# Kernel optimization log

Measured on AMD Instinct MI355X. Metric: run time of the kernel, lower is better.

Reference implementation:

```python
import jax, jax.numpy as jnp
import numpy as np

B, N = 8, 6                 # batch, cameras
D, C = 45, 64               # depth bins, context channels
FH, FW = 8, 22              # feature-map height/width
GX, GY, GZ = 64, 64, 32     # BEV grid: W, H, D in the torch code
RES = 0.5
XOFF, YOFF, ZOFF = 16.0, 16.0, 8.0


def _frustum():
    # matches LSS.create_frustum: pixel coords over full 352x128 image, depths 1..45
    xs = jnp.linspace(0.0, 351.0, FW)
    ys = jnp.linspace(0.0, 127.0, FH)
    ds = jnp.arange(1.0, 46.0, 1.0)
    d, y, x = jnp.meshgrid(ds, ys, xs, indexing='ij')   # [D, FH, FW]
    return jnp.stack([x * d, y * d, d], axis=-1)         # [D, FH, FW, 3]


def setup_inputs() -> dict:
    key = jax.random.key(0)
    k1, k2, k3 = jax.random.split(key, 3)
    # depthNet output: softmax over depth bins
    depth = jax.nn.softmax(jax.random.normal(k1, (B, N, D, FH, FW), dtype=jnp.float32), axis=2)
    feature = jax.random.normal(k2, (B, N, C, FH, FW), dtype=jnp.float32)
    # realistic pinhole intrinsics (invertible), identity rotations, small translations
    K = jnp.array([[250.0, 0.0, 176.0], [0.0, 250.0, 64.0], [0.0, 0.0, 1.0]], dtype=jnp.float32)
    intrinsics = jnp.tile(K, (B, N, 1, 1))
    rots = jnp.tile(jnp.eye(3, dtype=jnp.float32), (B, N, 1, 1))
    trans = jax.random.normal(k3, (B, N, 3), dtype=jnp.float32) * 0.5
    return {"depth": depth, "feature": feature, "rots": rots, "trans": trans, "intrinsics": intrinsics}


def reference(depth, feature, rots, trans, intrinsics):
    fr = _frustum()                                              # [D, FH, FW, 3]
    # get_geometry: unproject frustum to world
    inv_K = jnp.linalg.inv(intrinsics)                           # [B, N, 3, 3]
    pts_c = jnp.einsum('bnij,dhwj->bndhwi', inv_K, fr)           # camera frame
    geom = jnp.einsum('bnij,bndhwj->bndhwi', rots, pts_c) + trans[:, :, None, None, None, :]

    # context = depth outer-product feature: [B, N, D, C, FH, FW] -> [B,N,D,FH,FW,C]
    ctx = (depth[:, :, :, None] * feature[:, :, None]).transpose(0, 1, 2, 4, 5, 3)
    ctx = ctx.reshape(-1, C)                                     # [P, C]
    g = geom.reshape(-1, 3)                                      # [P, 3]

    # voxel index compute (astype int truncates toward zero, matching torch .long())
    nx = ((g[:, 0] + XOFF) / RES).astype(jnp.int32)
    ny = ((g[:, 2] + YOFF) / RES).astype(jnp.int32)
    nz = ((g[:, 1] + ZOFF) / RES).astype(jnp.int32)
    valid = (nx >= 0) & (nx < GX) & (ny >= 0) & (ny < GY) & (nz >= 0) & (nz < GZ)

    bidx = jnp.repeat(jnp.arange(B, dtype=jnp.int32), N * D * FH * FW)
    idx = jnp.where(valid, bidx * (GX * GY * GZ) + nx * (GY * GZ) + ny * GZ + nz, 0)

    # scatter-sum into dense BEV grid; invalid points contribute zero
    bev = jnp.zeros((B * GX * GY * GZ, C), dtype=ctx.dtype)
    bev = bev.at[idx].add(ctx * valid[:, None].astype(ctx.dtype))
    # [B, GX, GY, GZ, C] -> [B, C, GZ, GX, GY]
    return bev.reshape(B, GX, GY, GZ, C).transpose(0, 4, 3, 1, 2)
```

## Files before the change

kernel.cpp:

```cpp
#include <hip/hip_runtime.h>

#define BB 8
#define NN 6
#define DD 45
#define CC 64
#define FHH 8
#define FWW 22
#define GXX 64
#define GYY 64
#define GZZ 32
#define NPOINTS (BB*NN*DD*FHH*FWW)
#define NSITES (BB*NN*FHH*FWW)
#define ROWS (BB*GZZ)
#define NBINS (GXX*GYY)
#define CAPR 8192
#define HWSZ (FHH*FWW)

typedef float f32x4 __attribute__((ext_vector_type(4)));

#define WS_HIST_OFF 0
#define WS_OFF_OFF  ((size_t)ROWS * NBINS * 4)
#define WS_CUR_OFF  (WS_OFF_OFF + (size_t)ROWS * 4097 * 4)
#define WS_SORT_OFF (WS_CUR_OFF + (size_t)ROWS * NBINS * 4)
#define WS_FEATG_OFF (WS_SORT_OFF + (size_t)ROWS * CAPR * 8)
#define WS_NEEDED (WS_FEATG_OFF + (size_t)16 * NSITES * 16)

__device__ __forceinline__ bool geom(int p, int& row, int& nxny, int& site, float& dv,
                                     const float* __restrict__ depth,
                                     const float* __restrict__ rots,
                                     const float* __restrict__ trans,
                                     const float* __restrict__ intr)
{
    int w = p % FWW;
    int t = p / FWW;
    int h = t % FHH; t /= FHH;
    int di = t % DD; t /= DD;
    int n = t % NN;
    int b = t / NN;

    float d = (float)(di + 1);
    float x = (float)(351.0 * (double)w / 21.0);
    float y = (float)(127.0 * (double)h / 7.0);

    const float* K = intr + (b * NN + n) * 9;
    double k00 = K[0], k01 = K[1], k02 = K[2];
    double k10 = K[3], k11 = K[4], k12 = K[5];
    double k20 = K[6], k21 = K[7], k22 = K[8];
    double det = k00 * (k11 * k22 - k12 * k21)
               - k01 * (k10 * k22 - k12 * k20)
               + k02 * (k10 * k21 - k11 * k20);
    double id = 1.0 / det;
    float i00 = (float)(( k11 * k22 - k12 * k21) * id);
    float i01 = (float)((-k01 * k22 + k02 * k21) * id);
    float i02 = (float)(( k01 * k12 - k02 * k11) * id);
    float i10 = (float)((-k10 * k22 + k12 * k20) * id);
    float i11 = (float)(( k00 * k22 - k02 * k20) * id);
    float i12 = (float)((-k00 * k12 + k02 * k10) * id);
    float i20 = (float)(( k10 * k21 - k11 * k20) * id);
    float i21 = (float)((-k00 * k21 + k01 * k20) * id);
    float i22 = (float)(( k00 * k11 - k01 * k10) * id);

    float p0 = x * d, p1 = y * d, p2 = d;
    float c0 = i00 * p0 + i01 * p1 + i02 * p2;
    float c1 = i10 * p0 + i11 * p1 + i12 * p2;
    float c2 = i20 * p0 + i21 * p1 + i22 * p2;

    const float* R = rots + (b * NN + n) * 9;
    const float* T = trans + (b * NN + n) * 3;
    float g0 = R[0] * c0 + R[1] * c1 + R[2] * c2 + T[0];
    float g1 = R[3] * c0 + R[4] * c1 + R[5] * c2 + T[1];
    float g2 = R[6] * c0 + R[7] * c1 + R[8] * c2 + T[2];

    int nx = (int)((g0 + 16.0f) / 0.5f);
    int ny = (int)((g2 + 16.0f) / 0.5f);
    int nz = (int)((g1 + 8.0f)  / 0.5f);
    bool valid = (nx >= 0) & (nx < GXX) & (ny >= 0) & (ny < GYY) & (nz >= 0) & (nz < GZZ);

    row  = (b * GZZ + nz);
    nxny = (nx << 6) | ny;
    site = ((b * NN + n) * FHH + h) * FWW + w;
    dv = depth[p];
    return valid;
}

__global__ __launch_bounds__(256) void lss_prep(const float* __restrict__ feature,
                                                int* __restrict__ hist,
                                                float4* __restrict__ featG) {
    int i = blockIdx.x * 256 + threadIdx.x;
    int stride = gridDim.x * 256;
    for (int k = i; k < ROWS * NBINS; k += stride) hist[k] = 0;
    for (int k = i; k < 16 * NSITES; k += stride) {
        int site = k % NSITES;
        int ccb = k / NSITES;
        int hw = site % HWSZ;
        int cam = site / HWSZ;
        const float* fb = feature + ((size_t)cam * CC + ccb * 4) * HWSZ + hw;
        featG[k] = make_float4(fb[0], fb[HWSZ], fb[2 * HWSZ], fb[3 * HWSZ]);
    }
}

__global__ __launch_bounds__(256) void lss_build1(
    const float* __restrict__ depth, const float* __restrict__ rots,
    const float* __restrict__ trans, const float* __restrict__ intr,
    int* __restrict__ hist)
{
    int p = blockIdx.x * 256 + threadIdx.x;
    int row, nxny, site; float dv;
    if (geom(p, row, nxny, site, dv, depth, rots, trans, intr))
        atomicAdd(&hist[row * NBINS + nxny], 1);
}

__global__ __launch_bounds__(256) void lss_scan(const int* __restrict__ hist,
                                                int* __restrict__ off,
                                                int* __restrict__ cur) {
    int row = blockIdx.x;
    const int* h = hist + row * NBINS;
    int* o = off + row * 4097;
    int* cu = cur + row * NBINS;
    int tid = threadIdx.x;

    int vals[16]; int sum = 0;
    #pragma unroll
    for (int i = 0; i < 16; ++i) { vals[i] = sum; sum += h[tid * 16 + i]; }

    __shared__ int ts[256];
    ts[tid] = sum;
    __syncthreads();
    for (int ofs = 1; ofs < 256; ofs <<= 1) {
        int v = (tid >= ofs) ? ts[tid - ofs] : 0;
        __syncthreads();
        ts[tid] += v;
        __syncthreads();
    }
    int base = tid ? ts[tid - 1] : 0;
    #pragma unroll
    for (int i = 0; i < 16; ++i) {
        int val = base + vals[i];
        o[tid * 16 + i] = val;
        cu[tid * 16 + i] = val;
    }
    if (tid == 255) o[4096] = ts[255];
}

__global__ __launch_bounds__(256) void lss_build2(
    const float* __restrict__ depth, const float* __restrict__ rots,
    const float* __restrict__ trans, const float* __restrict__ intr,
    int* __restrict__ cur, int2* __restrict__ sorted)
{
    int p = blockIdx.x * 256 + threadIdx.x;
    int row, nxny, site; float dv;
    if (geom(p, row, nxny, site, dv, depth, rots, trans, intr)) {
        int pos = atomicAdd(&cur[row * NBINS + nxny], 1);
        sorted[(size_t)row * CAPR + pos] = make_int2(__float_as_int(dv), (site << 12) | nxny);
    }
}

__global__ __launch_bounds__(256) void lss_out8(
    const float4* __restrict__ featG,
    const int* __restrict__ cnt_row,
    const int2* __restrict__ sorted,
    float* __restrict__ out)
{
    int bid = blockIdx.x;
    int ccb = bid & 15;
    int row = bid >> 4;
    int b = row >> 5, nz = row & 31;
    int tid = threadIdx.x;

    int scnt = cnt_row[row];
    if (scnt > CAPR) scnt = CAPR;

    size_t ob0 = (((size_t)b * CC + ccb * 4) * GZZ + nz) * (GXX * GYY);
    const size_t cstride = (size_t)GZZ * GXX * GYY;

    if (scnt == 0) {
        f32x4 z = (f32x4){0.f, 0.f, 0.f, 0.f};
        #pragma unroll
        for (int cc = 0; cc < 4; ++cc) {
            f32x4* op = (f32x4*)(out + ob0 + (size_t)cc * cstride);
            #pragma unroll
            for (int k = 0; k < 4; ++k) op[tid + k * 256] = z;
        }
        return;
    }

    __shared__ float acc[4 * NBINS];
    {
        f32x4 z = (f32x4){0.f, 0.f, 0.f, 0.f};
        f32x4* a4 = (f32x4*)acc;
        #pragma unroll
        for (int k = 0; k < 16; ++k) a4[tid + k * 256] = z;
    }
    __syncthreads();

    const float4* fg = featG + (size_t)ccb * NSITES;
    const int2* bk = sorted + (size_t)row * CAPR;

    int E = (scnt + 255) >> 8;
    int s0 = tid * E;
    int e0 = s0 + E; if (e0 > scnt) e0 = scnt;

    f32x4 racc = (f32x4){0.f, 0.f, 0.f, 0.f};
    int rvox = -1;
    for (int e = s0; e < e0; ++e) {
        int2 en = bk[e];
        int meta = en.y;
        int vox = meta & 4095;
        float dv = __int_as_float(en.x);
        float4 f = fg[meta >> 12];
        if (vox != rvox) {
            if (rvox >= 0) {
                atomicAdd(&acc[0 * NBINS + rvox], racc.x);
                atomicAdd(&acc[1 * NBINS + rvox], racc.y);
                atomicAdd(&acc[2 * NBINS + rvox], racc.z);
                atomicAdd(&acc[3 * NBINS + rvox], racc.w);
            }
            rvox = vox;
            racc = (f32x4){0.f, 0.f, 0.f, 0.f};
        }
        racc.x += dv * f.x;
        racc.y += dv * f.y;
        racc.z += dv * f.z;
        racc.w += dv * f.w;
    }
    if (rvox >= 0) {
        atomicAdd(&acc[0 * NBINS + rvox], racc.x);
        atomicAdd(&acc[1 * NBINS + rvox], racc.y);
        atomicAdd(&acc[2 * NBINS + rvox], racc.z);
        atomicAdd(&acc[3 * NBINS + rvox], racc.w);
    }
    __syncthreads();

    #pragma unroll
    for (int cc = 0; cc < 4; ++cc) {
        const f32x4* a4 = (const f32x4*)(acc + cc * NBINS);
        f32x4* op = (f32x4*)(out + ob0 + (size_t)cc * cstride);
        for (int i = tid; i < 1024; i += 256)
            op[i] = a4[i];
    }
}

__global__ __launch_bounds__(256) void lss_rowcnt(const int* __restrict__ off,
                                                  int* __restrict__ cnt_row) {
    int r = blockIdx.x * 256 + threadIdx.x;
    if (r < ROWS) cnt_row[r] = off[r * 4097 + 4096];
}

__global__ __launch_bounds__(256) void lss_zero(float4* __restrict__ p, int n4) {
    int i = blockIdx.x * blockDim.x + threadIdx.x;
    int stride = gridDim.x * blockDim.x;
    float4 z = make_float4(0.f, 0.f, 0.f, 0.f);
    for (; i < n4; i += stride) p[i] = z;
}

__global__ __launch_bounds__(256) void lss_scatter_direct(
    const float* __restrict__ depth, const float* __restrict__ feature,
    const float* __restrict__ rots, const float* __restrict__ trans,
    const float* __restrict__ intr, float* __restrict__ out)
{
    int p = blockIdx.x * 4 + (threadIdx.x >> 6);
    int lane = threadIdx.x & 63;
    int row, nxny, site; float dv;
    if (!geom(p, row, nxny, site, dv, depth, rots, trans, intr)) return;
    int b = row >> 5, nz = row & 31;
    int nx = nxny >> 6, ny = nxny & 63;
    int cam = site / HWSZ;
    float fv = feature[((size_t)cam * CC + lane) * HWSZ + (site % HWSZ)];
    size_t oidx = ((((size_t)b * CC + lane) * GZZ + nz) * GXX + nx) * GYY + ny;
    atomicAdd(out + oidx, dv * fv);
}

extern "C" void kernel_launch(void* const* d_in, const int* in_sizes, int n_in,
                              void* d_out, int out_size, void* d_ws, size_t ws_size,
                              hipStream_t stream) {
    const float* depth   = (const float*)d_in[0];
    const float* feature = (const float*)d_in[1];
    const float* rots    = (const float*)d_in[2];
    const float* trans   = (const float*)d_in[3];
    const float* intr    = (const float*)d_in[4];
    float* out = (float*)d_out;

    if (ws_size >= WS_NEEDED + 4096) {
        int*    hist   = (int*)((char*)d_ws + WS_HIST_OFF);
        int*    off    = (int*)((char*)d_ws + WS_OFF_OFF);
        int*    cur    = (int*)((char*)d_ws + WS_CUR_OFF);
        int2*   sorted = (int2*)((char*)d_ws + WS_SORT_OFF);
        float4* featG  = (float4*)((char*)d_ws + WS_FEATG_OFF);
        int*    cnt_row = (int*)((char*)d_ws + WS_NEEDED);

        lss_prep<<<4096, 256, 0, stream>>>(feature, hist, featG);
        lss_build1<<<NPOINTS / 256, 256, 0, stream>>>(depth, rots, trans, intr, hist);
        lss_scan<<<ROWS, 256, 0, stream>>>(hist, off, cur);
        lss_rowcnt<<<1, 256, 0, stream>>>(off, cnt_row);
        lss_build2<<<NPOINTS / 256, 256, 0, stream>>>(depth, rots, trans, intr, cur, sorted);
        lss_out8<<<ROWS * 16, 256, 0, stream>>>(featG, cnt_row, sorted, out);
    } else {
        lss_zero<<<4096, 256, 0, stream>>>((float4*)out, out_size / 4);
        lss_scatter_direct<<<NPOINTS / 4, 256, 0, stream>>>(depth, feature, rots, trans, intr, out);
    }
}
```

Before: 83.99 us.

## Cache voxel keys from histogram pass and drop separate cursor and rowcount kernels

The first build pass now stores each point's packed row/voxel key in a workspace array, so the second pass reads it instead of recomputing the camera geometry. The offsets array itself serves as the atomic cursor, which removes the separate cursor copy. The row-count kernel is folded into the scan, the histogram zeroing is vectorised, and the prep grid is shrunk. This trades an extra per-point write and read for less arithmetic and one fewer launch.

```diff
diff --git a/kernel.cpp b/kernel.cpp
--- a/kernel.cpp
+++ b/kernel.cpp
@@ -20,13 +20,13 @@
 
 #define WS_HIST_OFF 0
 #define WS_OFF_OFF  ((size_t)ROWS * NBINS * 4)
-#define WS_CUR_OFF  (WS_OFF_OFF + (size_t)ROWS * 4097 * 4)
-#define WS_SORT_OFF (WS_CUR_OFF + (size_t)ROWS * NBINS * 4)
+#define WS_REC_OFF  (WS_OFF_OFF + (size_t)ROWS * 4097 * 4)
+#define WS_SORT_OFF (WS_REC_OFF + (size_t)NPOINTS * 4)
 #define WS_FEATG_OFF (WS_SORT_OFF + (size_t)ROWS * CAPR * 8)
-#define WS_NEEDED (WS_FEATG_OFF + (size_t)16 * NSITES * 16)
-
-__device__ __forceinline__ bool geom(int p, int& row, int& nxny, int& site, float& dv,
-                                     const float* __restrict__ depth,
+#define WS_CNTR_OFF (WS_FEATG_OFF + (size_t)16 * NSITES * 16)
+#define WS_NEEDED (WS_CNTR_OFF + (size_t)ROWS * 4)
+
+__device__ __forceinline__ bool geom(int p, int& row, int& nxny,
                                      const float* __restrict__ rots,
                                      const float* __restrict__ trans,
                                      const float* __restrict__ intr)
@@ -78,8 +78,6 @@
 
     row  = (b * GZZ + nz);
     nxny = (nx << 6) | ny;
-    site = ((b * NN + n) * FHH + h) * FWW + w;
-    dv = depth[p];
     return valid;
 }
 
@@ -88,7 +86,9 @@
                                                 float4* __restrict__ featG) {
     int i = blockIdx.x * 256 + threadIdx.x;
     int stride = gridDim.x * 256;
-    for (int k = i; k < ROWS * NBINS; k += stride) hist[k] = 0;
+    int4* h4 = (int4*)hist;
+    int4 z4 = make_int4(0, 0, 0, 0);
+    for (int k = i; k < ROWS * NBINS / 4; k += stride) h4[k] = z4;
     for (int k = i; k < 16 * NSITES; k += stride) {
         int site = k % NSITES;
         int ccb = k / NSITES;
@@ -100,23 +100,26 @@
 }
 
 __global__ __launch_bounds__(256) void lss_build1(
-    const float* __restrict__ depth, const float* __restrict__ rots,
-    const float* __restrict__ trans, const float* __restrict__ intr,
-    int* __restrict__ hist)
+    const float* __restrict__ rots, const float* __restrict__ trans,
+    const float* __restrict__ intr,
+    int* __restrict__ rec, int* __restrict__ hist)
 {
     int p = blockIdx.x * 256 + threadIdx.x;
-    int row, nxny, site; float dv;
-    if (geom(p, row, nxny, site, dv, depth, rots, trans, intr))
+    int row, nxny;
+    if (geom(p, row, nxny, rots, trans, intr)) {
+        rec[p] = (row << 12) | nxny;
         atomicAdd(&hist[row * NBINS + nxny], 1);
+    } else {
+        rec[p] = -1;
+    }
 }
 
 __global__ __launch_bounds__(256) void lss_scan(const int* __restrict__ hist,
                                                 int* __restrict__ off,
-                                                int* __restrict__ cur) {
+                                                int* __restrict__ cnt_row) {
     int row = blockIdx.x;
     const int* h = hist + row * NBINS;
     int* o = off + row * 4097;
-    int* cu = cur + row * NBINS;
     int tid = threadIdx.x;
 
     int vals[16]; int sum = 0;
@@ -134,25 +137,29 @@
     }
     int base = tid ? ts[tid - 1] : 0;
     #pragma unroll
-    for (int i = 0; i < 16; ++i) {
-        int val = base + vals[i];
-        o[tid * 16 + i] = val;
-        cu[tid * 16 + i] = val;
-    }
-    if (tid == 255) o[4096] = ts[255];
+    for (int i = 0; i < 16; ++i)
+        o[tid * 16 + i] = base + vals[i];
+    if (tid == 255) { o[4096] = ts[255]; cnt_row[row] = ts[255]; }
 }
 
 __global__ __launch_bounds__(256) void lss_build2(
-    const float* __restrict__ depth, const float* __restrict__ rots,
-    const float* __restrict__ trans, const float* __restrict__ intr,
-    int* __restrict__ cur, int2* __restrict__ sorted)
+    const float* __restrict__ depth, const int* __restrict__ rec,
+    int* __restrict__ off, int2* __restrict__ sorted)
 {
     int p = blockIdx.x * 256 + threadIdx.x;
-    int row, nxny, site; float dv;
-    if (geom(p, row, nxny, site, dv, depth, rots, trans, intr)) {
-        int pos = atomicAdd(&cur[row * NBINS + nxny], 1);
+    int r = rec[p];
+    if (r < 0) return;
+    int row = r >> 12;
+    int nxny = r & 4095;
+    int w = p % FWW;
+    int t = p / FWW;
+    int h = t % FHH; t /= FHH;
+    int cam = t / DD;
+    int site = (cam * FHH + h) * FWW + w;
+    float dv = depth[p];
+    int pos = atomicAdd(&off[row * 4097 + nxny], 1);
+    if (pos < CAPR)
         sorted[(size_t)row * CAPR + pos] = make_int2(__float_as_int(dv), (site << 12) | nxny);
-    }
 }
 
 __global__ __launch_bounds__(256) void lss_out8(
@@ -240,12 +247,6 @@
     }
 }
 
-__global__ __launch_bounds__(256) void lss_rowcnt(const int* __restrict__ off,
-                                                  int* __restrict__ cnt_row) {
-    int r = blockIdx.x * 256 + threadIdx.x;
-    if (r < ROWS) cnt_row[r] = off[r * 4097 + 4096];
-}
-
 __global__ __launch_bounds__(256) void lss_zero(float4* __restrict__ p, int n4) {
     int i = blockIdx.x * blockDim.x + threadIdx.x;
     int stride = gridDim.x * blockDim.x;
@@ -260,12 +261,16 @@
 {
     int p = blockIdx.x * 4 + (threadIdx.x >> 6);
     int lane = threadIdx.x & 63;
-    int row, nxny, site; float dv;
-    if (!geom(p, row, nxny, site, dv, depth, rots, trans, intr)) return;
+    int row, nxny;
+    if (!geom(p, row, nxny, rots, trans, intr)) return;
     int b = row >> 5, nz = row & 31;
     int nx = nxny >> 6, ny = nxny & 63;
-    int cam = site / HWSZ;
-    float fv = feature[((size_t)cam * CC + lane) * HWSZ + (site % HWSZ)];
+    int w = p % FWW;
+    int t = p / FWW;
+    int h = t % FHH; t /= FHH;
+    int cam = t / DD;
+    float dv = depth[p];
+    float fv = feature[((size_t)cam * CC + lane) * HWSZ + h * FWW + w];
     size_t oidx = ((((size_t)b * CC + lane) * GZZ + nz) * GXX + nx) * GYY + ny;
     atomicAdd(out + oidx, dv * fv);
 }
@@ -280,19 +285,18 @@
     const float* intr    = (const float*)d_in[4];
     float* out = (float*)d_out;
 
-    if (ws_size >= WS_NEEDED + 4096) {
-        int*    hist   = (int*)((char*)d_ws + WS_HIST_OFF);
-        int*    off    = (int*)((char*)d_ws + WS_OFF_OFF);
-        int*    cur    = (int*)((char*)d_ws + WS_CUR_OFF);
-        int2*   sorted = (int2*)((char*)d_ws + WS_SORT_OFF);
-        float4* featG  = (float4*)((char*)d_ws + WS_FEATG_OFF);
-        int*    cnt_row = (int*)((char*)d_ws + WS_NEEDED);
-
-        lss_prep<<<4096, 256, 0, stream>>>(feature, hist, featG);
-        lss_build1<<<NPOINTS / 256, 256, 0, stream>>>(depth, rots, trans, intr, hist);
-        lss_scan<<<ROWS, 256, 0, stream>>>(hist, off, cur);
-        lss_rowcnt<<<1, 256, 0, stream>>>(off, cnt_row);
-        lss_build2<<<NPOINTS / 256, 256, 0, stream>>>(depth, rots, trans, intr, cur, sorted);
+    if (ws_size >= WS_NEEDED) {
+        int*    hist    = (int*)((char*)d_ws + WS_HIST_OFF);
+        int*    off     = (int*)((char*)d_ws + WS_OFF_OFF);
+        int*    rec     = (int*)((char*)d_ws + WS_REC_OFF);
+        int2*   sorted  = (int2*)((char*)d_ws + WS_SORT_OFF);
+        float4* featG   = (float4*)((char*)d_ws + WS_FEATG_OFF);
+        int*    cnt_row = (int*)((char*)d_ws + WS_CNTR_OFF);
+
+        lss_prep<<<1024, 256, 0, stream>>>(feature, hist, featG);
+        lss_build1<<<NPOINTS / 256, 256, 0, stream>>>(rots, trans, intr, rec, hist);
+        lss_scan<<<ROWS, 256, 0, stream>>>(hist, off, cnt_row);
+        lss_build2<<<NPOINTS / 256, 256, 0, stream>>>(depth, rec, off, sorted);
         lss_out8<<<ROWS * 16, 256, 0, stream>>>(featG, cnt_row, sorted, out);
     } else {
         lss_zero<<<4096, 256, 0, stream>>>((float4*)out, out_size / 4);
```

Result: faster. 79.46 us (-5.4%).
